# Kernel optimization log

Measured on AMD Instinct MI355X. Metric: run time of the kernel, lower is better.

The kernel has to match this reference:

```python
import jax, jax.numpy as jnp
from jax import lax
import numpy as np

BATCH, SEQ_LEN, ENC_IN, C_OUT = 16, 512, 32, 32
N_ORDER = 256           # window_size
MULTISCALE = (1, 2, 4)
MODES = min(32, SEQ_LEN // 2)  # = 32


def make_hippo(N, dt):
    """HiPPO-LegT transition, bilinear (Tustin) discretization, Legendre eval matrix."""
    Q = np.arange(N, dtype=np.float64)
    R = (2 * Q + 1)[:, None]
    j, i = np.meshgrid(Q, Q)
    A = np.where(i < j, -1.0, (-1.0) ** (i - j + 1)) * R
    B = (-1.0) ** Q[:, None] * R                      # [N,1]
    I = np.eye(N)
    M = I - (dt / 2.0) * A
    Ad = np.linalg.solve(M, I + (dt / 2.0) * A)
    Bd = np.linalg.solve(M, dt * B).squeeze(-1)       # [N]
    vals = np.arange(0.0, 1.0, dt)
    x = 1.0 - 2.0 * vals
    P = np.zeros((N, len(vals)))
    P[0] = 1.0
    if N > 1:
        P[1] = x
    for n in range(1, N - 1):
        P[n + 1] = ((2 * n + 1) * x * P[n] - n * P[n - 1]) / (n + 1)
    E = P.T                                           # [len(vals), N]
    return Ad.astype(np.float32), Bd.astype(np.float32), E.astype(np.float32)


def setup_inputs():
    key = jax.random.key(0)
    ks = jax.random.split(key, 12)
    inp = {}
    inp['x_enc'] = jax.random.normal(ks[0], (BATCH, SEQ_LEN, ENC_IN), jnp.float32)
    inp['x_mark_enc'] = jax.random.normal(ks[1], (BATCH, SEQ_LEN, 4), jnp.float32)
    inp['x_dec'] = jax.random.normal(ks[2], (BATCH, SEQ_LEN, ENC_IN), jnp.float32)
    inp['x_mark_dec'] = jax.random.normal(ks[3], (BATCH, SEQ_LEN, 4), jnp.float32)
    inp['affine_weight'] = jnp.ones((1, 1, ENC_IN), jnp.float32)
    inp['affine_bias'] = jnp.zeros((1, 1, ENC_IN), jnp.float32)
    scale = 1.0 / (N_ORDER * N_ORDER)
    for s in range(3):
        inp[f'wr{s}'] = scale * jax.random.uniform(ks[4 + 2 * s], (N_ORDER, N_ORDER, MODES), jnp.float32)
        inp[f'wi{s}'] = scale * jax.random.uniform(ks[5 + 2 * s], (N_ORDER, N_ORDER, MODES), jnp.float32)
    inp['mlp_w'] = 0.1 * jax.random.normal(ks[10], (1, 3), jnp.float32)
    inp['mlp_b'] = jnp.zeros((1,), jnp.float32)
    inp['proj_w'] = 0.02 * jax.random.normal(ks[11], (ENC_IN, C_OUT), jnp.float32)
    inp['proj_b'] = jnp.zeros((C_OUT,), jnp.float32)
    for s, m in enumerate(MULTISCALE):
        A, Bv, E = make_hippo(N_ORDER, 1.0 / SEQ_LEN / m)
        inp[f'A{s}'] = jnp.asarray(A)
        inp[f'Bv{s}'] = jnp.asarray(Bv)
        inp[f'E{s}'] = jnp.asarray(E)
    return inp


def _hippo_scan(x, A, Bv):
    # x: [B, L, C] -> cs: [L, B, C, N]; c_t = A c_{t-1} + B f_t (applied on last dim)
    B_, L, C = x.shape
    c0 = jnp.zeros((B_, C, A.shape[0]), x.dtype)
    At = A.T
    def step(c, f):                      # f: [B, C]
        c = c @ At + f[..., None] * Bv
        return c, c
    _, cs = lax.scan(step, c0, jnp.transpose(x, (1, 0, 2)))
    return cs


def _spectral_conv(xc, wr, wi):
    # xc: [B, C, N, L]; keep first MODES rfft bins, complex channel mix over N, irfft
    L = xc.shape[-1]
    xf = jnp.fft.rfft(xc)                                # [B,C,N,L//2+1] complex64
    W = (wr + 1j * wi).astype(jnp.complex64)             # [N,N,MODES]
    out = jnp.einsum('bjix,iox->bjox', xf[..., :MODES], W)
    out_ft = jnp.pad(out, ((0, 0), (0, 0), (0, 0), (0, L // 2 + 1 - MODES)))
    return jnp.fft.irfft(out_ft, n=L)                    # [B,C,N,L]


def _forward(x_enc, affine_weight, affine_bias, specs, mlp_w, mlp_b, proj_w, proj_b, hippos):
    means = lax.stop_gradient(jnp.mean(x_enc, axis=1, keepdims=True))
    xc = x_enc - means
    stdev = lax.stop_gradient(jnp.sqrt(jnp.var(xc, axis=1, keepdims=True) + 1e-5))
    x = xc / stdev
    x = x * affine_weight + affine_bias                  # [B, L, C]
    pred_len = SEQ_LEN
    decs = []
    for (wr, wi), (A, Bv, E) in zip(specs, hippos):
        # multiscale slice x[:, -m*pred_len:] clips to full seq_len since pred_len==seq_len
        cs = _hippo_scan(x, A, Bv)                       # [L,B,C,N]
        x_in_c = jnp.transpose(cs, (1, 2, 3, 0))         # [B,C,N,L]
        out1 = _spectral_conv(x_in_c, wr, wi)            # [B,C,N,L]
        x_dec_c = out1[..., pred_len - 1]                # [B,C,N]
        dec = x_dec_c @ E[-pred_len:, :].T               # [B,C,pred_len]
        decs.append(dec)
    stacked = jnp.stack(decs, axis=-1)                   # [B,C,P,3]
    y = stacked @ mlp_w[0] + mlp_b[0]                    # Linear(3,1) + squeeze -> [B,C,P]
    y = jnp.transpose(y, (0, 2, 1))                      # [B,P,C]
    y = (y - affine_bias) / (affine_weight + 1e-10)
    y = y * stdev + means
    return y @ proj_w + proj_b                           # OutputBlock: per-step channel projection


def reference(x_enc, x_mark_enc, x_dec, x_mark_dec, affine_weight, affine_bias,
              wr0, wi0, wr1, wi1, wr2, wi2, mlp_w, mlp_b, proj_w, proj_b,
              A0, Bv0, E0, A1, Bv1, E1, A2, Bv2, E2):
    specs = [(wr0, wi0), (wr1, wi1), (wr2, wi2)]
    hippos = [(A0, Bv0, E0), (A1, Bv1, E1), (A2, Bv2, E2)]
    return _forward(x_enc, affine_weight, affine_bias, specs, mlp_w, mlp_b, proj_w, proj_b, hippos)
```

## Files before the change

### kernel.cpp

```cpp
#include <hip/hip_runtime.h>
#include <math.h>

#define SEQ 512
#define NORD 256
#define MODES 32
#define KBIG (NORD*MODES*2)
#define PI_F 3.14159265358979323846f

typedef _Float16 half8 __attribute__((ext_vector_type(8)));
typedef float floatx4 __attribute__((ext_vector_type(4)));
typedef unsigned int uint;



struct GJob {
  const float* A; const float* B; float* C; const float* scale_ptr;
  int M, N, lda, k0, k1, atomic;
};
struct GJobs {
  GJob j[6];
  const float* wwr[3]; const float* wwi[3];
  _Float16* Wt; int nGemm; int wb_i0; int wb_slab0;
};

__global__ __launch_bounds__(256) void gemm32_k(GJobs P) {
  int z = blockIdx.z;
  if (z >= P.nGemm) {
    if (blockIdx.y != 0) return;
    int ig = P.wb_i0 + (z - P.nGemm);
    int s = ig >> 8, i = ig & 255;
    const float* wr = P.wwr[s];
    const float* wi = P.wwi[s];
    uint* Wd = (uint*)(P.Wt + (size_t)(s - P.wb_slab0) * 4194304);
    int j = blockIdx.x * 256 + threadIdx.x;
    int ot = j >> 7, loc = j & 127;
    int ks = loc >> 6, kg8 = (loc >> 4) & 3, on = loc & 15;
    int o = ot * 16 + on, k0 = ks * 16 + kg8 * 4;
    float4 wr4 = *(const float4*)&wr[(size_t)i * 8192 + o * 32 + k0];
    float4 wi4 = *(const float4*)&wi[(size_t)i * 8192 + o * 32 + k0];
    float wa[4] = {wr4.x, wr4.y, wr4.z, wr4.w};
    float wb[4] = {wi4.x, wi4.y, wi4.z, wi4.w};
    uint out[4];
    #pragma unroll
    for (int q = 0; q < 4; q++) {
      int k = k0 + q;
      float sn, cn; __sincosf((2.f * PI_F / 512.f) * (float)k, &sn, &cn);
      float g = ((k == 0) ? (1.f / 512.f) : (2.f / 512.f)) * 4096.f;
      float v0 = g * (cn * wa[q] + sn * wb[q]);
      float v1 = g * (sn * wa[q] - cn * wb[q]);
      _Float16 h0 = (_Float16)v0, h1 = (_Float16)v1;
      unsigned short u0, u1;
      __builtin_memcpy(&u0, &h0, 2); __builtin_memcpy(&u1, &h1, 2);
      out[q] = (uint)u0 | ((uint)u1 << 16);
    }
    *(uint4*)&Wd[((size_t)(i * 16 + ot)) * 512 + loc * 4] = *(uint4*)out;
    return;
  }
  GJob jb = P.j[z];
  int col0 = blockIdx.x * 32;
  int row0 = blockIdx.y * 32;
  if (row0 >= jb.M || col0 >= jb.N) return;
  __shared__ float As[64][34];
  __shared__ float Bs[64][36];
  int tid = threadIdx.x;
  int tx = tid & 15, ty = tid >> 4;
  const float* A = jb.A; const float* B = jb.B;
  int M = jb.M, N = jb.N, lda = jb.lda;
  int kcA = (tid & 15) * 4, rA = tid >> 4;
  int ccB = (tid & 7) * 4, kkB = tid >> 3;
  int gr0 = row0 + rA, gr1 = row0 + rA + 16;
  const float4 z4 = make_float4(0.f, 0.f, 0.f, 0.f);
  float4 a0, a1, b0, b1;
  {
    int kb = jb.k0;
    a0 = (gr0 < M) ? *(const float4*)&A[(size_t)gr0 * lda + kb + kcA] : z4;
    a1 = (gr1 < M) ? *(const float4*)&A[(size_t)gr1 * lda + kb + kcA] : z4;
    b0 = *(const float4*)&B[(size_t)(kb + kkB) * N + col0 + ccB];
    b1 = *(const float4*)&B[(size_t)(kb + kkB + 32) * N + col0 + ccB];
  }
  float acc00 = 0.f, acc01 = 0.f, acc10 = 0.f, acc11 = 0.f;
  for (int kb = jb.k0; kb < jb.k1; kb += 64) {
    As[kcA+0][rA] = a0.x; As[kcA+1][rA] = a0.y; As[kcA+2][rA] = a0.z; As[kcA+3][rA] = a0.w;
    As[kcA+0][rA+16] = a1.x; As[kcA+1][rA+16] = a1.y; As[kcA+2][rA+16] = a1.z; As[kcA+3][rA+16] = a1.w;
    *(float4*)&Bs[kkB][ccB] = b0;
    *(float4*)&Bs[kkB+32][ccB] = b1;
    __syncthreads();
    if (kb + 64 < jb.k1) {
      int kn = kb + 64;
      a0 = (gr0 < M) ? *(const float4*)&A[(size_t)gr0 * lda + kn + kcA] : z4;
      a1 = (gr1 < M) ? *(const float4*)&A[(size_t)gr1 * lda + kn + kcA] : z4;
      b0 = *(const float4*)&B[(size_t)(kn + kkB) * N + col0 + ccB];
      b1 = *(const float4*)&B[(size_t)(kn + kkB + 32) * N + col0 + ccB];
    }
    #pragma unroll
    for (int k = 0; k < 64; k++) {
      float2 av = *(float2*)&As[k][ty * 2];
      float2 bv = *(float2*)&Bs[k][tx * 2];
      acc00 += av.x * bv.x; acc01 += av.x * bv.y;
      acc10 += av.y * bv.x; acc11 += av.y * bv.y;
    }
    __syncthreads();
  }
  float sc = jb.scale_ptr ? *jb.scale_ptr : 1.f;
  int gr = row0 + ty * 2, gc = col0 + tx * 2;
  float v00 = acc00 * sc, v01 = acc01 * sc, v10 = acc10 * sc, v11 = acc11 * sc;
  if (jb.atomic) {
    if (gr < M)     { atomicAdd(&jb.C[(size_t)gr * N + gc], v00);     atomicAdd(&jb.C[(size_t)gr * N + gc + 1], v01); }
    if (gr + 1 < M) { atomicAdd(&jb.C[(size_t)(gr+1) * N + gc], v10); atomicAdd(&jb.C[(size_t)(gr+1) * N + gc + 1], v11); }
  } else {
    if (gr < M)     { jb.C[(size_t)gr * N + gc] = v00;     jb.C[(size_t)gr * N + gc + 1] = v01; }
    if (gr + 1 < M) { jb.C[(size_t)(gr+1) * N + gc] = v10; jb.C[(size_t)(gr+1) * N + gc + 1] = v11; }
  }
}


__global__ __launch_bounds__(256) void setup_k(const float* A0, const float* A1, const float* A2,
                                               const float* B0, const float* B1, const float* B2,
                                               const float* E0, const float* E1, const float* E2,
                                               const float* x, const float* aw, const float* ab,
                                               float* R, float* Kry, float* Et, float* Z,
                                               float* F, float* stats) {
  long bid = blockIdx.x;
  int tid = threadIdx.x;
  if (bid < 768) {
    long idx = bid * 256 + tid;
    int scl = (int)(idx >> 16);
    int r = (int)(idx & 65535);
    int m = r >> 8, i2 = r & 255;
    const float* A = scl == 0 ? A0 : (scl == 1 ? A1 : A2);
    R[(size_t)scl * 2 * 65536 + (size_t)m * 256 + i2] = A[(size_t)i2 * 256 + m];
  } else if (bid < 2304) {
    long idx = (bid - 768) * 256 + tid;
    int scl = (int)(idx / 131072);
    int r = (int)(idx % 131072);
    int p = r >> 8, o = r & 255;
    const float* E; int rows;
    if (scl == 0) { E = E0; rows = 512; }
    else if (scl == 1) { E = E1; rows = 1024; }
    else { E = E2; rows = 2048; }
    int base = rows - 512;
    Et[(size_t)scl * 131072 + (size_t)o * 512 + p] = E[(size_t)(base + p) * 256 + o];
  } else if (bid < 2307) {
    int scl = (int)(bid - 2304);
    const float* B = scl == 0 ? B0 : (scl == 1 ? B1 : B2);
    Kry[(size_t)scl * 131072 + tid] = B[tid];
  } else if (bid < 3843) {
    long idx = (bid - 2307) * 256 + tid;
    Z[idx] = 0.f;
  } else {
    int row = (int)(bid - 3843);
    int b = row >> 5, c = row & 31;
    const float* xp = x + (size_t)b * SEQ * 32 + c;
    float v0 = xp[(size_t)tid * 32];
    float v1 = xp[(size_t)(tid + 256) * 32];
    float s = v0 + v1, s2 = v0 * v0 + v1 * v1;
    for (int off = 32; off; off >>= 1) {
      s  += __shfl_down(s,  off, 64);
      s2 += __shfl_down(s2, off, 64);
    }
    __shared__ float ws1[4], ws2[4];
    __shared__ float mean_s, istd_s;
    int wid = tid >> 6, lane = tid & 63;
    if (lane == 0) { ws1[wid] = s; ws2[wid] = s2; }
    __syncthreads();
    if (tid == 0) {
      float t1 = ws1[0] + ws1[1] + ws1[2] + ws1[3];
      float t2 = ws2[0] + ws2[1] + ws2[2] + ws2[3];
      float mean = t1 / 512.f;
      float var = t2 / 512.f - mean * mean;
      float sd = sqrtf(var + 1e-5f);
      mean_s = mean; istd_s = 1.f / sd;
      stats[row] = mean; stats[512 + row] = sd;
    }
    __syncthreads();
    float w = aw[c], bb = ab[c];
    float m = mean_s, is = istd_s;
    F[(size_t)row * SEQ + tid]       = (v0 - m) * is * w + bb;
    F[(size_t)row * SEQ + tid + 256] = (v1 - m) * is * w + bb;
  }
}


__global__ __launch_bounds__(256) void qbuildA_k(const float* __restrict__ Kry,
                                                 float2* __restrict__ Pp, int s0) {
  int bg = blockIdx.x;
  int s = s0 + (bg >> 8);
  int r = bg & 255;
  int k = r & 31, c = r >> 5;
  const float* Kry_s = Kry + (size_t)s * 131072;
  float2* P = Pp + (size_t)s * 65536;
  int i = threadIdx.x;
  float ar = 0.f, ai = 0.f;
  const float step = 2.f * PI_F / 512.f;
  int m0 = c * 64;
  for (int mm = 0; mm < 64; mm++) {
    int m = m0 + mm;
    float kap = Kry_s[(size_t)m * 256 + i];
    float sn, cn; __sincosf(step * (float)((k * m) & 511), &sn, &cn);
    ar += kap * cn; ai -= kap * sn;
  }
  P[(size_t)(c * 32 + k) * 256 + i] = make_float2(ar, ai);
}


__global__ __launch_bounds__(256) void qbuildB_k(const float* __restrict__ Kry,
                                                 const float2* __restrict__ Pp,
                                                 _Float16* __restrict__ Qf, int s0) {
  int bg = blockIdx.x;
  int slab = bg >> 8;
  int s = s0 + slab;
  int r = bg & 255;
  int ig = r & 31, c = r >> 5;
  const float* Kry_s = Kry + (size_t)s * 131072;
  const float2* P = Pp + (size_t)s * 65536;
  uint* Qd = (uint*)(Qf + (size_t)slab * 8388608);
  int tid = threadIdx.x;
  int k = tid & 31, il = tid >> 5;
  int i = ig * 8 + il;
  __shared__ __align__(16) uint buf[16 * 260];
  float ar = 0.f, ai = 0.f;
  for (int cp = 0; cp < c; cp++) {
    float2 p = P[(size_t)(cp * 32 + k) * 256 + i];
    ar += p.x; ai += p.y;
  }
  const float step = 2.f * PI_F / 512.f;
  int m0 = c * 64;
  int u = tid & 31, myil = tid >> 5;
  for (int mb = 0; mb < 64; mb += 16) {
    #pragma unroll
    for (int mm = 0; mm < 16; mm++) {
      int m = m0 + mb + mm;
      float kap = Kry_s[(size_t)m * 256 + i];
      float sn, cn; __sincosf(step * (float)((k * m) & 511), &sn, &cn);
      ar += kap * cn; ai -= kap * sn;
      int st = 511 - m;
      float sn2, cn2; __sincosf(step * (float)((k * st) & 511), &sn2, &cn2);
      float qr = ar * cn2 + ai * sn2;
      float qi = ai * cn2 - ar * sn2;
      qr = fminf(fmaxf(qr, -60000.f), 60000.f);
      qi = fminf(fmaxf(qi, -60000.f), 60000.f);
      _Float16 h0 = (_Float16)qr, h1 = (_Float16)qi;
      unsigned short u0, u1;
      __builtin_memcpy(&u0, &h0, 2); __builtin_memcpy(&u1, &h1, 2);
      buf[(st & 15) * 260 + il * 32 + k] = (uint)u0 | ((uint)u1 << 16);
    }
    __syncthreads();
    int stt = (511 - (m0 + mb)) >> 4;
    int kc = ig * 8 + myil;
    uint* tile = Qd + ((size_t)(kc * 32 + stt)) * 512;
    #pragma unroll
    for (int r4 = 0; r4 < 4; r4++) {
      int f = u * 4 + r4;
      int m = f & 15, kg8 = (f >> 4) & 3, ks = f >> 6;
      uint4 v = *(uint4*)&buf[m * 260 + myil * 32 + ks * 16 + kg8 * 4];
      *(uint4*)&tile[f * 4] = v;
    }
    __syncthreads();
  }
}


__global__ __launch_bounds__(256, 3) void umfma_k(const _Float16* __restrict__ Qf,
                                                  const _Float16* __restrict__ Wt,
                                                  float* __restrict__ U, int nGrp) {
  __shared__ __align__(16) uint Al_u[4096];
  __shared__ __align__(16) uint Bl_u[4096];
  int Fb = blockIdx.x;
  int xcd = Fb & 7, jj = Fb >> 3;
  int g = (jj >> 3) * 8 + xcd;
  int mem = jj & 7;
  if (g >= nGrp) return;
  int slab = g >> 5, ks = g & 31;
  int mx = mem & 3, ny = mem >> 2;
  const uint* Qt = (const uint*)(Qf + (size_t)slab * 8388608);
  const uint* Wu = (const uint*)(Wt + (size_t)slab * 4194304);
  float* Us = U + (size_t)slab * 131072;
  int stt0 = mx * 8, ot0 = ny * 8;
  int m0 = mx * 128, n0 = ny * 128;
  int tid = threadIdx.x;
  int w = tid >> 6, lane = tid & 63;
  int quad = lane >> 4, lm = lane & 15;
  floatx4 acc[4][4];
  #pragma unroll
  for (int a = 0; a < 4; a++)
    #pragma unroll
    for (int b = 0; b < 4; b++) acc[a][b] = (floatx4)(0.f);
  int wmt = (w & 1) * 4, wnt = (w >> 1) * 4;
  uint4 qa[4], qb[4];
  {
    int kc = ks * 8;
    const uint* qsrc = Qt + ((size_t)(kc * 32 + stt0)) * 512;
    const uint* wsrc = Wu + ((size_t)(kc * 16 + ot0)) * 512;
    #pragma unroll
    for (int r = 0; r < 4; r++) {
      qa[r] = *(const uint4*)&qsrc[(r * 256 + tid) * 4];
      qb[r] = *(const uint4*)&wsrc[(r * 256 + tid) * 4];
    }
  }
  for (int it = 0; it < 8; it++) {
    __syncthreads();
    #pragma unroll
    for (int r = 0; r < 4; r++) {
      *(uint4*)&Al_u[(r * 256 + tid) * 4] = qa[r];
      *(uint4*)&Bl_u[(r * 256 + tid) * 4] = qb[r];
    }
    __syncthreads();
    if (it < 7) {
      int kc = ks * 8 + it + 1;
      const uint* qsrc = Qt + ((size_t)(kc * 32 + stt0)) * 512;
      const uint* wsrc = Wu + ((size_t)(kc * 16 + ot0)) * 512;
      #pragma unroll
      for (int r = 0; r < 4; r++) {
        qa[r] = *(const uint4*)&qsrc[(r * 256 + tid) * 4];
        qb[r] = *(const uint4*)&wsrc[(r * 256 + tid) * 4];
      }
    }
    #pragma unroll
    for (int kss = 0; kss < 2; kss++) {
      half8 af[4], bf[4];
      #pragma unroll
      for (int t = 0; t < 4; t++) {
        af[t] = *(half8*)((_Float16*)Al_u + ((wmt + t) * 1024 + kss * 512 + lane * 8));
        bf[t] = *(half8*)((_Float16*)Bl_u + ((wnt + t) * 1024 + kss * 512 + lane * 8));
      }
      #pragma unroll
      for (int mi = 0; mi < 4; mi++)
        #pragma unroll
        for (int ni = 0; ni < 4; ni++)
          acc[mi][ni] = __builtin_amdgcn_mfma_f32_16x16x32_f16(af[mi], bf[ni], acc[mi][ni], 0, 0, 0);
    }
  }
  #pragma unroll
  for (int mi = 0; mi < 4; mi++) {
    int gr0 = m0 + wmt * 16 + mi * 16 + quad * 4;
    #pragma unroll
    for (int ni = 0; ni < 4; ni++) {
      int gc = n0 + wnt * 16 + ni * 16 + lm;
      #pragma unroll
      for (int r = 0; r < 4; r++)
        atomicAdd(&Us[(size_t)(gr0 + r) * 256 + gc], acc[mi][ni][r] * (1.f / 4096.f));
    }
  }
}


__global__ __launch_bounds__(256) void y0final_k(const float* __restrict__ F,
                                                 const float* __restrict__ Ttot,
                                                 const float* __restrict__ stats,
                                                 const float* __restrict__ aw,
                                                 const float* __restrict__ ab,
                                                 const float* __restrict__ mlp_b,
                                                 const float* __restrict__ pw,
                                                 const float* __restrict__ pb,
                                                 float* __restrict__ out) {
  __shared__ float As[64][34];
  __shared__ float Bs[64][36];
  __shared__ float ys[32][33];
  __shared__ float pws[1024];
  int bxp = blockIdx.x;
  int b = blockIdx.y;
  int row0 = b * 32, col0 = bxp * 32;
  int tid = threadIdx.x;
  for (int t = tid; t < 1024; t += 256) pws[t] = pw[t];
  int tx = tid & 15, ty = tid >> 4;
  int kcA = (tid & 15) * 4, rA = tid >> 4;
  int ccB = (tid & 7) * 4, kkB = tid >> 3;
  int gr0 = row0 + rA, gr1 = row0 + rA + 16;
  float4 a0, a1, b0, b1;
  a0 = *(const float4*)&F[(size_t)gr0 * 512 + kcA];
  a1 = *(const float4*)&F[(size_t)gr1 * 512 + kcA];
  b0 = *(const float4*)&Ttot[(size_t)kkB * 512 + col0 + ccB];
  b1 = *(const float4*)&Ttot[(size_t)(kkB + 32) * 512 + col0 + ccB];
  float acc00 = 0.f, acc01 = 0.f, acc10 = 0.f, acc11 = 0.f;
  for (int kb = 0; kb < 512; kb += 64) {
    As[kcA+0][rA] = a0.x; As[kcA+1][rA] = a0.y; As[kcA+2][rA] = a0.z; As[kcA+3][rA] = a0.w;
    As[kcA+0][rA+16] = a1.x; As[kcA+1][rA+16] = a1.y; As[kcA+2][rA+16] = a1.z; As[kcA+3][rA+16] = a1.w;
    *(float4*)&Bs[kkB][ccB] = b0;
    *(float4*)&Bs[kkB+32][ccB] = b1;
    __syncthreads();
    if (kb + 64 < 512) {
      int kn = kb + 64;
      a0 = *(const float4*)&F[(size_t)gr0 * 512 + kn + kcA];
      a1 = *(const float4*)&F[(size_t)gr1 * 512 + kn + kcA];
      b0 = *(const float4*)&Ttot[(size_t)(kn + kkB) * 512 + col0 + ccB];
      b1 = *(const float4*)&Ttot[(size_t)(kn + kkB + 32) * 512 + col0 + ccB];
    }
    #pragma unroll
    for (int k = 0; k < 64; k++) {
      float2 av = *(float2*)&As[k][ty * 2];
      float2 bv = *(float2*)&Bs[k][tx * 2];
      acc00 += av.x * bv.x; acc01 += av.x * bv.y;
      acc10 += av.y * bv.x; acc11 += av.y * bv.y;
    }
    __syncthreads();
  }
  float mb0 = mlp_b[0];
  {
    int c0 = ty * 2, c1 = ty * 2 + 1;
    int r0g = row0 + c0, r1g = row0 + c1;
    float mean0 = stats[r0g], sd0 = stats[512 + r0g];
    float mean1 = stats[r1g], sd1 = stats[512 + r1g];
    float q0 = sd0 / (aw[c0] + 1e-10f), q1 = sd1 / (aw[c1] + 1e-10f);
    float o0 = mean0 - (ab[c0] - mb0) * q0, o1 = mean1 - (ab[c1] - mb0) * q1;
    ys[c0][tx * 2]     = acc00 * q0 + o0;
    ys[c0][tx * 2 + 1] = acc01 * q0 + o0;
    ys[c1][tx * 2]     = acc10 * q1 + o1;
    ys[c1][tx * 2 + 1] = acc11 * q1 + o1;
  }
  __syncthreads();
  int p = tid >> 3, co0 = (tid & 7) * 4;
  float4 facc = *(const float4*)&pb[co0];
  #pragma unroll
  for (int cc = 0; cc < 32; cc++) {
    float f = ys[cc][p];
    float4 pw4 = *(float4*)&pws[cc * 32 + co0];
    facc.x += f * pw4.x; facc.y += f * pw4.y; facc.z += f * pw4.z; facc.w += f * pw4.w;
  }
  *(float4*)&out[(size_t)b * 16384 + (size_t)(col0 + p) * 32 + co0] = facc;
}


extern "C" void kernel_launch(void* const* d_in, const int* in_sizes, int n_in,
                              void* d_out, int out_size, void* d_ws, size_t ws_size,
                              hipStream_t stream) {
  const float* x_enc = (const float*)d_in[0];
  const float* aw = (const float*)d_in[4];
  const float* ab = (const float*)d_in[5];
  const float* wr[3] = {(const float*)d_in[6], (const float*)d_in[8], (const float*)d_in[10]};
  const float* wi[3] = {(const float*)d_in[7], (const float*)d_in[9], (const float*)d_in[11]};
  const float* mlp_w = (const float*)d_in[12];
  const float* mlp_b = (const float*)d_in[13];
  const float* proj_w = (const float*)d_in[14];
  const float* proj_b = (const float*)d_in[15];
  const float* Am[3]  = {(const float*)d_in[16], (const float*)d_in[19], (const float*)d_in[22]};
  const float* Bv[3]  = {(const float*)d_in[17], (const float*)d_in[20], (const float*)d_in[23]};
  const float* Em[3]  = {(const float*)d_in[18], (const float*)d_in[21], (const float*)d_in[24]};

  float* w = (float*)d_ws;
  float* F     = w; w += 512 * 512;
  float* stats = w; w += 1024;
  float* Kry   = w; w += 3 * 131072;
  float* R     = w; w += 3 * 2 * 65536;
  float* U     = w; w += 3 * 131072;
  float* Ttot  = w; w += 512 * 512;
  float* Et    = w; w += 3 * 131072;
  float* Pp    = w; w += 3 * 131072;
  _Float16* Qf = (_Float16*)w;

  size_t base_bytes = (size_t)((char*)Qf - (char*)d_ws);
  size_t slab_bytes = (size_t)(8388608 + 4194304) * 2;
  int nS = (ws_size >= base_bytes + 3 * slab_bytes) ? 3 : 1;
  _Float16* Wb = Qf + (size_t)nS * 8388608;

  setup_k<<<4355, 256, 0, stream>>>(Am[0], Am[1], Am[2], Bv[0], Bv[1], Bv[2],
                                    Em[0], Em[1], Em[2], x_enc, aw, ab,
                                    R, Kry, Et, U, F, stats);

  int wb_done = 0;
  for (int j = 0; j < 9; j++) {
    GJobs P{};
    int M = 1 << j;
    int cur = j & 1;
    int nz = 0;
    for (int s = 0; s < 3; s++) {
      float* Ks = Kry + (size_t)s * 131072;
      float* Rj = R + (size_t)s * 131072 + (size_t)cur * 65536;
      float* Rn = R + (size_t)s * 131072 + (size_t)(1 - cur) * 65536;
      P.j[nz++] = {Ks, Rj, Ks + (size_t)M * 256, nullptr, M, 256, 256, 0, 256, 0};
      if (j < 8) P.j[nz++] = {Rj, Rj, Rn, nullptr, 256, 256, 256, 0, 256, 0};
    }
    P.nGemm = nz;
    int wb_cnt = 0;
    if (nS == 3) {
      wb_cnt = (j < 8) ? 86 : (768 - 86 * 8);
      P.wwr[0] = wr[0]; P.wwr[1] = wr[1]; P.wwr[2] = wr[2];
      P.wwi[0] = wi[0]; P.wwi[1] = wi[1]; P.wwi[2] = wi[2];
      P.Wt = Wb; P.wb_i0 = wb_done; P.wb_slab0 = 0;
      wb_done += wb_cnt;
    }
    gemm32_k<<<dim3(8, 8, nz + wb_cnt), 256, 0, stream>>>(P);
  }

  if (nS == 3) {
    qbuildA_k<<<768, 256, 0, stream>>>(Kry, (float2*)Pp, 0);
    qbuildB_k<<<768, 256, 0, stream>>>(Kry, (const float2*)Pp, Qf, 0);
    umfma_k<<<768, 256, 0, stream>>>(Qf, Wb, U, 96);
  } else {
    for (int s = 0; s < 3; s++) {
      GJobs P{};
      P.nGemm = 0;
      P.wwr[0] = wr[0]; P.wwr[1] = wr[1]; P.wwr[2] = wr[2];
      P.wwi[0] = wi[0]; P.wwi[1] = wi[1]; P.wwi[2] = wi[2];
      P.Wt = Wb; P.wb_i0 = s * 256; P.wb_slab0 = s;
      gemm32_k<<<dim3(8, 1, 256), 256, 0, stream>>>(P);
      qbuildA_k<<<256, 256, 0, stream>>>(Kry, (float2*)Pp, s);
      qbuildB_k<<<256, 256, 0, stream>>>(Kry, (const float2*)Pp, Qf, s);
      umfma_k<<<256, 256, 0, stream>>>(Qf, Wb, U + 0, 32);
    }
  }

  {
    GJobs P{};
    for (int s = 0; s < 3; s++)
      P.j[s] = {U + (size_t)s * 131072, Et + (size_t)s * 131072, Ttot,
                mlp_w + s, 512, 512, 256, 0, 256, 1};
    P.nGemm = 3;
    gemm32_k<<<dim3(16, 16, 3), 256, 0, stream>>>(P);
  }

  y0final_k<<<dim3(16, 16), 256, 0, stream>>>(F, Ttot, stats, aw, ab, mlp_b,
                                              proj_w, proj_b, (float*)d_out);
}
```

Baseline: 412.2 us.

## Replace atomic split-K accumulation with partial buffers plus reduction kernel

The MFMA kernel now writes each split-K partial tile into its own workspace slice, and a new reduce kernel sums them and applies the scale. This replaces the float atomicAdds into U and drops the zeroing pass in setup. The Ttot GEMM also stops accumulating across the three scales with atomics and uses a fused tile kernel that loops over the scales and stores once. The cost is roughly 50 MB of extra partial-buffer traffic and one more launch.

```diff
diff --git a/kernel.cpp b/kernel.cpp
--- a/kernel.cpp
+++ b/kernel.cpp
@@ -114,11 +114,54 @@
 }
 
 
+__device__ __forceinline__ void gemm_tile(const float* __restrict__ A,
+                                          const float* __restrict__ B,
+                                          int N, int lda, int K,
+                                          int row0, int col0, float ascale,
+                                          float (*As)[34], float (*Bs)[36],
+                                          float* acc) {
+  int tid = threadIdx.x;
+  int tx = tid & 15, ty = tid >> 4;
+  int kcA = (tid & 15) * 4, rA = tid >> 4;
+  int ccB = (tid & 7) * 4, kkB = tid >> 3;
+  int gr0 = row0 + rA, gr1 = row0 + rA + 16;
+  float4 a0, a1, b0, b1;
+  a0 = *(const float4*)&A[(size_t)gr0 * lda + kcA];
+  a1 = *(const float4*)&A[(size_t)gr1 * lda + kcA];
+  b0 = *(const float4*)&B[(size_t)kkB * N + col0 + ccB];
+  b1 = *(const float4*)&B[(size_t)(kkB + 32) * N + col0 + ccB];
+  for (int kb = 0; kb < K; kb += 64) {
+    As[kcA+0][rA] = a0.x * ascale; As[kcA+1][rA] = a0.y * ascale;
+    As[kcA+2][rA] = a0.z * ascale; As[kcA+3][rA] = a0.w * ascale;
+    As[kcA+0][rA+16] = a1.x * ascale; As[kcA+1][rA+16] = a1.y * ascale;
+    As[kcA+2][rA+16] = a1.z * ascale; As[kcA+3][rA+16] = a1.w * ascale;
+    *(float4*)&Bs[kkB][ccB] = b0;
+    *(float4*)&Bs[kkB+32][ccB] = b1;
+    __syncthreads();
+    if (kb + 64 < K) {
+      int kn = kb + 64;
+      a0 = *(const float4*)&A[(size_t)gr0 * lda + kn + kcA];
+      a1 = *(const float4*)&A[(size_t)gr1 * lda + kn + kcA];
+      b0 = *(const float4*)&B[(size_t)(kn + kkB) * N + col0 + ccB];
+      b1 = *(const float4*)&B[(size_t)(kn + kkB + 32) * N + col0 + ccB];
+    }
+    #pragma unroll
+    for (int k = 0; k < 64; k++) {
+      float2 av = *(float2*)&As[k][ty * 2];
+      float2 bv = *(float2*)&Bs[k][tx * 2];
+      acc[0] += av.x * bv.x; acc[1] += av.x * bv.y;
+      acc[2] += av.y * bv.x; acc[3] += av.y * bv.y;
+    }
+    __syncthreads();
+  }
+}
+
+
 __global__ __launch_bounds__(256) void setup_k(const float* A0, const float* A1, const float* A2,
                                                const float* B0, const float* B1, const float* B2,
                                                const float* E0, const float* E1, const float* E2,
                                                const float* x, const float* aw, const float* ab,
-                                               float* R, float* Kry, float* Et, float* Z,
+                                               float* R, float* Kry, float* Et,
                                                float* F, float* stats) {
   long bid = blockIdx.x;
   int tid = threadIdx.x;
@@ -144,11 +187,8 @@
     int scl = (int)(bid - 2304);
     const float* B = scl == 0 ? B0 : (scl == 1 ? B1 : B2);
     Kry[(size_t)scl * 131072 + tid] = B[tid];
-  } else if (bid < 3843) {
-    long idx = (bid - 2307) * 256 + tid;
-    Z[idx] = 0.f;
   } else {
-    int row = (int)(bid - 3843);
+    int row = (int)(bid - 2307);
     int b = row >> 5, c = row & 31;
     const float* xp = x + (size_t)b * SEQ * 32 + c;
     float v0 = xp[(size_t)tid * 32];
@@ -262,7 +302,8 @@
 
 __global__ __launch_bounds__(256, 3) void umfma_k(const _Float16* __restrict__ Qf,
                                                   const _Float16* __restrict__ Wt,
-                                                  float* __restrict__ U, int nGrp) {
+                                                  float* __restrict__ Pt,
+                                                  int nKs, int nGrp) {
   __shared__ __align__(16) uint Al_u[4096];
   __shared__ __align__(16) uint Bl_u[4096];
   int Fb = blockIdx.x;
@@ -270,11 +311,11 @@
   int g = (jj >> 3) * 8 + xcd;
   int mem = jj & 7;
   if (g >= nGrp) return;
-  int slab = g >> 5, ks = g & 31;
+  int slab = g / nKs, ks = g - slab * nKs;
   int mx = mem & 3, ny = mem >> 2;
   const uint* Qt = (const uint*)(Qf + (size_t)slab * 8388608);
   const uint* Wu = (const uint*)(Wt + (size_t)slab * 4194304);
-  float* Us = U + (size_t)slab * 131072;
+  float* Po = Pt + (size_t)g * 131072;
   int stt0 = mx * 8, ot0 = ny * 8;
   int m0 = mx * 128, n0 = ny * 128;
   int tid = threadIdx.x;
@@ -286,18 +327,19 @@
     #pragma unroll
     for (int b = 0; b < 4; b++) acc[a][b] = (floatx4)(0.f);
   int wmt = (w & 1) * 4, wnt = (w >> 1) * 4;
+  int nkc = 256 / nKs;
+  int kc0 = ks * nkc;
   uint4 qa[4], qb[4];
   {
-    int kc = ks * 8;
-    const uint* qsrc = Qt + ((size_t)(kc * 32 + stt0)) * 512;
-    const uint* wsrc = Wu + ((size_t)(kc * 16 + ot0)) * 512;
+    const uint* qsrc = Qt + ((size_t)(kc0 * 32 + stt0)) * 512;
+    const uint* wsrc = Wu + ((size_t)(kc0 * 16 + ot0)) * 512;
     #pragma unroll
     for (int r = 0; r < 4; r++) {
       qa[r] = *(const uint4*)&qsrc[(r * 256 + tid) * 4];
       qb[r] = *(const uint4*)&wsrc[(r * 256 + tid) * 4];
     }
   }
-  for (int it = 0; it < 8; it++) {
+  for (int it = 0; it < nkc; it++) {
     __syncthreads();
     #pragma unroll
     for (int r = 0; r < 4; r++) {
@@ -305,8 +347,8 @@
       *(uint4*)&Bl_u[(r * 256 + tid) * 4] = qb[r];
     }
     __syncthreads();
-    if (it < 7) {
-      int kc = ks * 8 + it + 1;
+    if (it < nkc - 1) {
+      int kc = kc0 + it + 1;
       const uint* qsrc = Qt + ((size_t)(kc * 32 + stt0)) * 512;
       const uint* wsrc = Wu + ((size_t)(kc * 16 + ot0)) * 512;
       #pragma unroll
@@ -338,9 +380,49 @@
       int gc = n0 + wnt * 16 + ni * 16 + lm;
       #pragma unroll
       for (int r = 0; r < 4; r++)
-        atomicAdd(&Us[(size_t)(gr0 + r) * 256 + gc], acc[mi][ni][r] * (1.f / 4096.f));
-    }
-  }
+        Po[(size_t)(gr0 + r) * 256 + gc] = acc[mi][ni][r];
+    }
+  }
+}
+
+
+__global__ __launch_bounds__(256) void reduce_k(const float* __restrict__ Pt,
+                                                float* __restrict__ U,
+                                                int nKs, int nSlab) {
+  int e4 = blockIdx.x * 256 + threadIdx.x;
+  int slab = e4 >> 15;
+  int rem = e4 & 32767;
+  if (slab >= nSlab) return;
+  const float4* base = (const float4*)Pt + (size_t)(slab * nKs) * 32768 + rem;
+  float4 a = make_float4(0.f, 0.f, 0.f, 0.f);
+  for (int ks = 0; ks < nKs; ks++) {
+    float4 v = base[(size_t)ks * 32768];
+    a.x += v.x; a.y += v.y; a.z += v.z; a.w += v.w;
+  }
+  const float sc = 1.f / 4096.f;
+  a.x *= sc; a.y *= sc; a.z *= sc; a.w *= sc;
+  ((float4*)U)[e4] = a;
+}
+
+
+__global__ __launch_bounds__(256) void ttot_k(const float* __restrict__ U,
+                                              const float* __restrict__ Et,
+                                              const float* __restrict__ mlp_w,
+                                              float* __restrict__ Ttot) {
+  __shared__ float As[64][34];
+  __shared__ float Bs[64][36];
+  int lt = blockIdx.x;
+  int rt = lt >> 4, ct = lt & 15;
+  int row0 = rt * 32, col0 = ct * 32;
+  float acc[4] = {0.f, 0.f, 0.f, 0.f};
+  for (int s = 0; s < 3; s++)
+    gemm_tile(U + (size_t)s * 131072, Et + (size_t)s * 131072,
+              512, 256, 256, row0, col0, mlp_w[s], As, Bs, acc);
+  int tid = threadIdx.x;
+  int tx = tid & 15, ty = tid >> 4;
+  int gr = row0 + ty * 2, gc = col0 + tx * 2;
+  Ttot[(size_t)gr * 512 + gc] = acc[0];       Ttot[(size_t)gr * 512 + gc + 1] = acc[1];
+  Ttot[(size_t)(gr+1) * 512 + gc] = acc[2];   Ttot[(size_t)(gr+1) * 512 + gc + 1] = acc[3];
 }
 
 
@@ -363,37 +445,8 @@
   int tid = threadIdx.x;
   for (int t = tid; t < 1024; t += 256) pws[t] = pw[t];
   int tx = tid & 15, ty = tid >> 4;
-  int kcA = (tid & 15) * 4, rA = tid >> 4;
-  int ccB = (tid & 7) * 4, kkB = tid >> 3;
-  int gr0 = row0 + rA, gr1 = row0 + rA + 16;
-  float4 a0, a1, b0, b1;
-  a0 = *(const float4*)&F[(size_t)gr0 * 512 + kcA];
-  a1 = *(const float4*)&F[(size_t)gr1 * 512 + kcA];
-  b0 = *(const float4*)&Ttot[(size_t)kkB * 512 + col0 + ccB];
-  b1 = *(const float4*)&Ttot[(size_t)(kkB + 32) * 512 + col0 + ccB];
-  float acc00 = 0.f, acc01 = 0.f, acc10 = 0.f, acc11 = 0.f;
-  for (int kb = 0; kb < 512; kb += 64) {
-    As[kcA+0][rA] = a0.x; As[kcA+1][rA] = a0.y; As[kcA+2][rA] = a0.z; As[kcA+3][rA] = a0.w;
-    As[kcA+0][rA+16] = a1.x; As[kcA+1][rA+16] = a1.y; As[kcA+2][rA+16] = a1.z; As[kcA+3][rA+16] = a1.w;
-    *(float4*)&Bs[kkB][ccB] = b0;
-    *(float4*)&Bs[kkB+32][ccB] = b1;
-    __syncthreads();
-    if (kb + 64 < 512) {
-      int kn = kb + 64;
-      a0 = *(const float4*)&F[(size_t)gr0 * 512 + kn + kcA];
-      a1 = *(const float4*)&F[(size_t)gr1 * 512 + kn + kcA];
-      b0 = *(const float4*)&Ttot[(size_t)(kn + kkB) * 512 + col0 + ccB];
-      b1 = *(const float4*)&Ttot[(size_t)(kn + kkB + 32) * 512 + col0 + ccB];
-    }
-    #pragma unroll
-    for (int k = 0; k < 64; k++) {
-      float2 av = *(float2*)&As[k][ty * 2];
-      float2 bv = *(float2*)&Bs[k][tx * 2];
-      acc00 += av.x * bv.x; acc01 += av.x * bv.y;
-      acc10 += av.y * bv.x; acc11 += av.y * bv.y;
-    }
-    __syncthreads();
-  }
+  float acc[4] = {0.f, 0.f, 0.f, 0.f};
+  gemm_tile(F, Ttot, 512, 512, 512, row0, col0, 1.f, As, Bs, acc);
   float mb0 = mlp_b[0];
   {
     int c0 = ty * 2, c1 = ty * 2 + 1;
@@ -402,10 +455,10 @@
     float mean1 = stats[r1g], sd1 = stats[512 + r1g];
     float q0 = sd0 / (aw[c0] + 1e-10f), q1 = sd1 / (aw[c1] + 1e-10f);
     float o0 = mean0 - (ab[c0] - mb0) * q0, o1 = mean1 - (ab[c1] - mb0) * q1;
-    ys[c0][tx * 2]     = acc00 * q0 + o0;
-    ys[c0][tx * 2 + 1] = acc01 * q0 + o0;
-    ys[c1][tx * 2]     = acc10 * q1 + o1;
-    ys[c1][tx * 2 + 1] = acc11 * q1 + o1;
+    ys[c0][tx * 2]     = acc[0] * q0 + o0;
+    ys[c0][tx * 2 + 1] = acc[1] * q0 + o0;
+    ys[c1][tx * 2]     = acc[2] * q1 + o1;
+    ys[c1][tx * 2 + 1] = acc[3] * q1 + o1;
   }
   __syncthreads();
   int p = tid >> 3, co0 = (tid & 7) * 4;
@@ -448,13 +501,24 @@
   _Float16* Qf = (_Float16*)w;
 
   size_t base_bytes = (size_t)((char*)Qf - (char*)d_ws);
-  size_t slab_bytes = (size_t)(8388608 + 4194304) * 2;
-  int nS = (ws_size >= base_bytes + 3 * slab_bytes) ? 3 : 1;
+  size_t qwb3 = (size_t)3 * (8388608 + 4194304) * 2;
+  size_t qwb1 = (size_t)(8388608 + 4194304) * 2;
+  size_t pt32 = (size_t)96 * 131072 * 4;
+  size_t pt16 = (size_t)48 * 131072 * 4;
+  size_t pt1  = (size_t)32 * 131072 * 4;
+
+  int mode;
+  if (ws_size >= base_bytes + qwb3 + pt32) mode = 2;
+  else if (ws_size >= base_bytes + qwb3 + pt16) mode = 1;
+  else mode = 0;
+
+  int nS = (mode > 0) ? 3 : 1;
   _Float16* Wb = Qf + (size_t)nS * 8388608;
-
-  setup_k<<<4355, 256, 0, stream>>>(Am[0], Am[1], Am[2], Bv[0], Bv[1], Bv[2],
+  float* Pt = (float*)(Wb + (size_t)nS * 4194304);
+
+  setup_k<<<2819, 256, 0, stream>>>(Am[0], Am[1], Am[2], Bv[0], Bv[1], Bv[2],
                                     Em[0], Em[1], Em[2], x_enc, aw, ab,
-                                    R, Kry, Et, U, F, stats);
+                                    R, Kry, Et, F, stats);
 
   int wb_done = 0;
   for (int j = 0; j < 9; j++) {
@@ -481,10 +545,12 @@
     gemm32_k<<<dim3(8, 8, nz + wb_cnt), 256, 0, stream>>>(P);
   }
 
-  if (nS == 3) {
+  if (mode > 0) {
+    int nKs = (mode == 2) ? 32 : 16;
     qbuildA_k<<<768, 256, 0, stream>>>(Kry, (float2*)Pp, 0);
     qbuildB_k<<<768, 256, 0, stream>>>(Kry, (const float2*)Pp, Qf, 0);
-    umfma_k<<<768, 256, 0, stream>>>(Qf, Wb, U, 96);
+    umfma_k<<<3 * nKs * 8, 256, 0, stream>>>(Qf, Wb, Pt, nKs, 3 * nKs);
+    reduce_k<<<384, 256, 0, stream>>>(Pt, U, nKs, 3);
   } else {
     for (int s = 0; s < 3; s++) {
       GJobs P{};
@@ -495,18 +561,12 @@
       gemm32_k<<<dim3(8, 1, 256), 256, 0, stream>>>(P);
       qbuildA_k<<<256, 256, 0, stream>>>(Kry, (float2*)Pp, s);
       qbuildB_k<<<256, 256, 0, stream>>>(Kry, (const float2*)Pp, Qf, s);
-      umfma_k<<<256, 256, 0, stream>>>(Qf, Wb, U + 0, 32);
-    }
-  }
-
-  {
-    GJobs P{};
-    for (int s = 0; s < 3; s++)
-      P.j[s] = {U + (size_t)s * 131072, Et + (size_t)s * 131072, Ttot,
-                mlp_w + s, 512, 512, 256, 0, 256, 1};
-    P.nGemm = 3;
-    gemm32_k<<<dim3(16, 16, 3), 256, 0, stream>>>(P);
-  }
+      umfma_k<<<256, 256, 0, stream>>>(Qf, Wb, Pt, 32, 32);
+      reduce_k<<<128, 256, 0, stream>>>(Pt, U + (size_t)s * 131072, 32, 1);
+    }
+  }
+
+  ttot_k<<<256, 256, 0, stream>>>(U, Et, mlp_w, Ttot);
 
   y0final_k<<<dim3(16, 16), 256, 0, stream>>>(F, Ttot, stats, aw, ab, mlp_b,
                                               proj_w, proj_b, (float*)d_out);
```

New measurement: 399.4 us. 3.1% less time.
